# Kernel optimization log

Hardware: AMD Instinct MI355X
Metric: run time of the kernel (lower is better)

The kernel has to match this reference:

```python
import jax, jax.numpy as jnp
import numpy as np

SCALING = 2.5
OFFSET = 0.0
TIME_LENGTH = 10.0
DT = 0.1
CUTOFF = TIME_LENGTH  # cutoff=None -> time_length
TIME_STEPS = int(TIME_LENGTH // DT) + 1  # == 100 (float floor: 10.0//0.1 == 99.0)
CENTERS = np.array([-1.75, -1.25, -0.75, -0.25, 0.25, 0.75, 1.25, 1.75], dtype=np.float32)


def setup_inputs() -> dict:
    key = jax.random.key(0)
    k1, = jax.random.split(key, 1)
    trace = jax.random.normal(k1, (1024, 128), dtype=jnp.float32)
    center = jnp.asarray(CENTERS)
    return {"trace": trace, "center": center, "dummy1": 0, "dummy2": 0}


def reference(trace, center, dummy1, dummy2):
    B = trace.shape[0]
    # times: [B, F*C] latency per (feature, center) pair
    times = SCALING * jnp.abs(trace[..., None] - center).reshape(B, -1)
    times = jnp.where((times < 0) | (times > CUTOFF), TIME_LENGTH + DT, times)
    times = times + OFFSET
    bins = (times / DT + 1).astype(jnp.int32)  # trunc == floor for positive values
    mask = bins < TIME_STEPS
    N = times.shape[1]
    bi = jnp.broadcast_to(jnp.arange(B)[:, None], (B, N))
    ni = jnp.broadcast_to(jnp.arange(N)[None, :], (B, N))
    bins_c = jnp.clip(bins, 0, TIME_STEPS - 1)
    vals = mask.astype(jnp.int32)
    # masked scatter-add into pre-zeroed dense spike tensor (COO to_dense sums dups)
    spikes = jnp.zeros((TIME_STEPS, B, N), dtype=jnp.int32).at[bins_c, bi, ni].add(vals)
    return spikes
```

## Files before the change

### kernel.cpp

```cpp
#include <hip/hip_runtime.h>
#include <hip/hip_bf16.h>


#define BB 1024
#define FF 128
#define CC 8
#define NN 1024
#define TT 100
#define TCHUNK 25

__global__ __launch_bounds__(256) void ARNOLD_ENC_52639119180424_kernel(
        const float* __restrict__ trace,
        const float* __restrict__ center,
        int* __restrict__ out) {
    const int b   = blockIdx.x;
    const int tc  = blockIdx.y;
    const int tid = threadIdx.x;
    const int n0  = tid << 2;
    const int f   = n0 >> 3;
    const int c0  = n0 & 7;

    const float x = trace[b * FF + f];

    int bins[4];
#pragma unroll
    for (int i = 0; i < 4; ++i) {
        float tms = 2.5f * fabsf(x - center[c0 + i]);
        int bin = -1;
        if (!(tms > 10.0f)) {
            int bb = (int)(tms / 0.1f + 1.0f);
            if (bb < TT) bin = bb;
        }
        bins[i] = bin;
    }

    int* outp = out + (size_t)b * NN + n0;
    const int tbase = tc * TCHUNK;
#pragma unroll
    for (int t = 0; t < TCHUNK; ++t) {
        const int ttime = tbase + t;
        int4 v;
        v.x = (bins[0] == ttime) ? 1 : 0;
        v.y = (bins[1] == ttime) ? 1 : 0;
        v.z = (bins[2] == ttime) ? 1 : 0;
        v.w = (bins[3] == ttime) ? 1 : 0;
        *(int4*)(outp + (size_t)ttime * ((size_t)BB * NN)) = v;
    }
}

extern "C" void kernel_launch(void* const* d_in, const int* in_sizes, int n_in,
                              void* d_out, int out_size, void* d_ws, size_t ws_size,
                              hipStream_t stream) {
    const float* trace  = (const float*)d_in[0];
    const float* center = (const float*)d_in[1];
    int* out = (int*)d_out;

    dim3 grid(BB, TT / TCHUNK);
    ARNOLD_ENC_52639119180424_kernel<<<grid, 256, 0, stream>>>(trace, center, out);
}
```

Before: 426.4 us.

## Split into bin-precompute kernel and linear streaming write kernel

Bins are now computed once per element into a compact uint8 workspace, and a second kernel streams the 400MB output linearly, plane by plane, with each thread reading precomputed bins. Each block's writes are contiguous instead of 25 stores strided by a full plane. This adds a second launch and small workspace reads, which should be cheap next to the dominant output write.

```diff
diff --git a/kernel.cpp b/kernel.cpp
--- a/kernel.cpp
+++ b/kernel.cpp
@@ -4,17 +4,19 @@
 
 #define BB 1024
 #define FF 128
-#define CC 8
 #define NN 1024
 #define TT 100
-#define TCHUNK 25
+#define GROUPS_PER_PLANE ((BB * NN) / 4)
+#define NGROUPS (TT * GROUPS_PER_PLANE)
+#define P2_BLOCKS 4096
+#define P2_THREADS 256
+#define P2_ITERS (NGROUPS / (P2_BLOCKS * P2_THREADS))
 
-__global__ __launch_bounds__(256) void ARNOLD_ENC_52639119180424_kernel(
+__global__ __launch_bounds__(256) void arnold_bins_kernel(
         const float* __restrict__ trace,
         const float* __restrict__ center,
-        int* __restrict__ out) {
+        uchar4* __restrict__ bins) {
     const int b   = blockIdx.x;
-    const int tc  = blockIdx.y;
     const int tid = threadIdx.x;
     const int n0  = tid << 2;
     const int f   = n0 >> 3;
@@ -22,29 +24,32 @@
 
     const float x = trace[b * FF + f];
 
-    int bins[4];
+    unsigned char v[4];
 #pragma unroll
     for (int i = 0; i < 4; ++i) {
         float tms = 2.5f * fabsf(x - center[c0 + i]);
-        int bin = -1;
-        if (!(tms > 10.0f)) {
-            int bb = (int)(tms / 0.1f + 1.0f);
-            if (bb < TT) bin = bb;
-        }
-        bins[i] = bin;
+        unsigned bb = (tms > 10.0f) ? 255u : (unsigned)(tms / 0.1f + 1.0f);
+        v[i] = (unsigned char)bb;
     }
+    bins[(b << 8) + tid] = make_uchar4(v[0], v[1], v[2], v[3]);
+}
 
-    int* outp = out + (size_t)b * NN + n0;
-    const int tbase = tc * TCHUNK;
+__global__ __launch_bounds__(256) void arnold_stream_kernel(
+        const uchar4* __restrict__ bins,
+        int4* __restrict__ out) {
+    const int base = blockIdx.x * (P2_ITERS * P2_THREADS) + threadIdx.x;
 #pragma unroll
-    for (int t = 0; t < TCHUNK; ++t) {
-        const int ttime = tbase + t;
+    for (int k = 0; k < P2_ITERS; ++k) {
+        const int g = base + k * P2_THREADS;
+        const int t = g >> 18;
+        const int p = g & (GROUPS_PER_PLANE - 1);
+        const uchar4 c = bins[p];
         int4 v;
-        v.x = (bins[0] == ttime) ? 1 : 0;
-        v.y = (bins[1] == ttime) ? 1 : 0;
-        v.z = (bins[2] == ttime) ? 1 : 0;
-        v.w = (bins[3] == ttime) ? 1 : 0;
-        *(int4*)(outp + (size_t)ttime * ((size_t)BB * NN)) = v;
+        v.x = (c.x == t) ? 1 : 0;
+        v.y = (c.y == t) ? 1 : 0;
+        v.z = (c.z == t) ? 1 : 0;
+        v.w = (c.w == t) ? 1 : 0;
+        out[g] = v;
     }
 }
 
@@ -53,8 +58,9 @@
                               hipStream_t stream) {
     const float* trace  = (const float*)d_in[0];
     const float* center = (const float*)d_in[1];
-    int* out = (int*)d_out;
+    uchar4* bins = (uchar4*)d_ws;
+    int4* out = (int4*)d_out;
 
-    dim3 grid(BB, TT / TCHUNK);
-    ARNOLD_ENC_52639119180424_kernel<<<grid, 256, 0, stream>>>(trace, center, out);
+    arnold_bins_kernel<<<BB, 256, 0, stream>>>(trace, center, bins);
+    arnold_stream_kernel<<<P2_BLOCKS, P2_THREADS, 0, stream>>>(bins, out);
 }
```

New measurement: 423.3 us. No clear change (-0.7%).
